# Performance work log

Hardware: AMD Instinct MI355X
Metric: run time of the kernel (lower is better)

The kernel has to match this reference:

```python
import jax, jax.numpy as jnp
import numpy as np

N = 100000   # nodes
E = 1600000  # edges (before self loops)
G = 256      # graphs in batch
F = 128      # feature_size
H = 128      # hidden_channels
L = 3        # num_layers - 1 GAT layers
NC1 = 10     # task1 classes
GF = 8       # graph_feature_size
EPS = 1e-5


def _bn_pack(key, C):
    kg, kb, km, kv = jax.random.split(key, 4)
    gamma = jax.random.uniform(kg, (C,), minval=0.5, maxval=1.5)
    beta = jax.random.normal(kb, (C,)) * 0.1
    mean = jax.random.normal(km, (C,)) * 0.1
    var = jax.random.uniform(kv, (C,), minval=0.5, maxval=1.5)
    return jnp.stack([gamma, beta, mean, var]).astype(jnp.float32)  # [4, C]


def setup_inputs() -> dict:
    key = jax.random.key(0)
    ks = jax.random.split(key, 24)
    x = jax.random.normal(ks[0], (N, F), dtype=jnp.float32)
    edge_index = jax.random.randint(ks[1], (2, E), 0, N)
    batch_ids = jnp.sort(jax.random.randint(ks[2], (N,), 0, G))
    graph_features = jax.random.normal(ks[3], (G, GF), dtype=jnp.float32)
    s = 0.05
    gat_W = jax.random.normal(ks[4], (L, F, H), dtype=jnp.float32) * s
    gat_att_src = jax.random.normal(ks[5], (L, H), dtype=jnp.float32) * s
    gat_att_dst = jax.random.normal(ks[6], (L, H), dtype=jnp.float32) * s
    gat_bias = jax.random.normal(ks[7], (L, H), dtype=jnp.float32) * 0.01
    bn_emb = _bn_pack(ks[8], H)
    bn_t1 = _bn_pack(ks[9], NC1)
    bn_comb = _bn_pack(ks[10], H + 5)
    fc1_w = jax.random.normal(ks[11], (H + 1, NC1), dtype=jnp.float32) * s
    fc1_b = jax.random.normal(ks[12], (NC1,), dtype=jnp.float32) * s
    fc2_w = jax.random.normal(ks[13], (H + 3, 2), dtype=jnp.float32) * s
    fc2_b = jax.random.normal(ks[14], (2,), dtype=jnp.float32) * s
    fc3a_w = jax.random.normal(ks[15], (H + 5, 4), dtype=jnp.float32) * s
    fc3a_b = jax.random.normal(ks[16], (4,), dtype=jnp.float32) * s
    fc3b_w = jax.random.normal(ks[17], (H + 5, 5), dtype=jnp.float32) * s
    fc3b_b = jax.random.normal(ks[18], (5,), dtype=jnp.float32) * s
    return dict(x=x, edge_index=edge_index, batch_ids=batch_ids,
                graph_features=graph_features, task=0,
                gat_W=gat_W, gat_att_src=gat_att_src, gat_att_dst=gat_att_dst,
                gat_bias=gat_bias, bn_emb=bn_emb, bn_t1=bn_t1, bn_comb=bn_comb,
                fc1_w=fc1_w, fc1_b=fc1_b, fc2_w=fc2_w, fc2_b=fc2_b,
                fc3a_w=fc3a_w, fc3a_b=fc3a_b, fc3b_w=fc3b_w, fc3b_b=fc3b_b)


def _bn_eval(x, pack):
    gamma, beta, mean, var = pack
    return (x - mean) * gamma * jax.lax.rsqrt(var + EPS) + beta


def _gat_layer(x, W, a_src, a_dst, b, src, dst):
    h = x @ W                              # [N, H]
    e_src = (h @ a_src)[src]               # [Etot]
    e_dst = (h @ a_dst)[dst]
    e = jax.nn.leaky_relu(e_src + e_dst, negative_slope=0.2)
    emax = jax.ops.segment_max(e, dst, num_segments=N)
    ee = jnp.exp(e - emax[dst])
    denom = jax.ops.segment_sum(ee, dst, num_segments=N)
    alpha = ee / denom[dst]                # edge softmax per destination node
    out = jax.ops.segment_sum(h[src] * alpha[:, None], dst, num_segments=N)
    return out + b


def _forward(x, edge_index, batch_ids, graph_features,
             gat_W, gat_att_src, gat_att_dst, gat_bias,
             bn_emb, bn_t1, bn_comb,
             fc1_w, fc1_b, fc2_w, fc2_b, fc3a_w, fc3a_b, fc3b_w, fc3b_b):
    loops = jnp.arange(N)
    src = jnp.concatenate([edge_index[0], loops])  # PyG GATConv adds self-loops
    dst = jnp.concatenate([edge_index[1], loops])
    for i in range(L):
        x = jax.nn.relu(_gat_layer(x, gat_W[i], gat_att_src[i], gat_att_dst[i],
                                   gat_bias[i], src, dst))
    # global mean pool over graphs
    sums = jax.ops.segment_sum(x, batch_ids, num_segments=G)
    cnt = jax.ops.segment_sum(jnp.ones((N,), x.dtype), batch_ids, num_segments=G)
    x = sums / jnp.maximum(cnt, 1.0)[:, None]
    x = _bn_eval(x, bn_emb)
    lev_lsb = graph_features[:, -1:]
    nx_feats = graph_features[:, -3:]
    out1 = jnp.concatenate([x, lev_lsb], axis=1) @ fc1_w + fc1_b
    out1 = _bn_eval(jax.nn.relu(out1), bn_t1)
    out2 = jax.nn.relu(jnp.concatenate([x, nx_feats], axis=1) @ fc2_w + fc2_b)
    pred2 = jnp.argmax(out2, axis=1)
    wf1 = graph_features[:, 2:3]
    wf2 = graph_features[:, 1:2]
    x3 = _bn_eval(jnp.concatenate([x, wf1, wf2, nx_feats], axis=1), bn_comb)
    b1 = x3 @ fc3a_w + fc3a_b              # [G, 4]
    b2 = x3 @ fc3b_w + fc3b_b              # [G, 5]
    m0 = (pred2 == 0)[:, None].astype(x.dtype)
    m1 = (pred2 == 1)[:, None].astype(x.dtype)
    out3 = jnp.concatenate([b1 * m0, b2 * m1], axis=1)  # [G, 9]
    return out1, out2, out3


def reference(x, edge_index, batch_ids, graph_features, task,
              gat_W, gat_att_src, gat_att_dst, gat_bias,
              bn_emb, bn_t1, bn_comb,
              fc1_w, fc1_b, fc2_w, fc2_b, fc3a_w, fc3a_b, fc3b_w, fc3b_b):
    return _forward(x, edge_index, batch_ids, graph_features,
                    gat_W, gat_att_src, gat_att_dst, gat_bias,
                    bn_emb, bn_t1, bn_comb,
                    fc1_w, fc1_b, fc2_w, fc2_b, fc3a_w, fc3a_b, fc3b_w, fc3b_b)
```

## Files before the change

kernel.cpp:

```cpp
#include <hip/hip_runtime.h>
#include <math.h>

#define Nn 100000
#define Ee 1600000
#define Mm (Ee + Nn)
#define Gg 256
#define EPSf 1e-5f
#define NB 391
#define EPB 4096
#define NEB 391
#define PCAP 8192

typedef _Float16 f16x8 __attribute__((ext_vector_type(8)));
typedef _Float16 half4_t __attribute__((ext_vector_type(4)));
typedef float f32x4 __attribute__((ext_vector_type(4)));


__global__ void k_prepW(const float* __restrict__ W, _Float16* __restrict__ Wt,
                        int* __restrict__ gtail) {
  int l = blockIdx.x;
  if (l < 3) {
    const float* w = W + (size_t)l * 16384;
    _Float16* wt = Wt + (size_t)l * 16384;
    for (int i = threadIdx.x; i < 16384; i += 256) {
      int k = i >> 7, c = i & 127;
      wt[c * 128 + k] = (_Float16)w[i];
    }
  } else {
    for (int i = threadIdx.x; i < NB; i += 256) gtail[i] = 0;
  }
}


__global__ __launch_bounds__(256) void k_bin(const int* __restrict__ src,
                                             const int* __restrict__ dst,
                                             int* __restrict__ gtail,
                                             int* __restrict__ pairs, int e) {
  __shared__ int lcnt[NB];
  __shared__ int lbase[NB];
  int t = threadIdx.x;
  for (int i = t; i < NB; i += 256) lcnt[i] = 0;
  __syncthreads();
  int base = blockIdx.x * EPB;
  int pk[EPB / 256], br[EPB / 256], bk[EPB / 256];
  #pragma unroll
  for (int i = 0; i < EPB / 256; ++i) {
    int idx = base + i * 256 + t;
    if (idx < e) {
      int d = dst[idx];
      pk[i] = (src[idx] << 8) | (d & 255);
      bk[i] = d >> 8;
      br[i] = atomicAdd(&lcnt[bk[i]], 1);
    } else br[i] = -1;
  }
  __syncthreads();
  for (int i = t; i < NB; i += 256)
    if (lcnt[i] > 0) lbase[i] = atomicAdd(&gtail[i], lcnt[i]);
  __syncthreads();
  #pragma unroll
  for (int i = 0; i < EPB / 256; ++i) {
    if (br[i] >= 0) {
      int pos = lbase[bk[i]] + br[i];
      if (pos < PCAP) pairs[bk[i] * PCAP + pos] = pk[i];
    }
  }
}

__global__ __launch_bounds__(256) void k_place(const int* __restrict__ pairs,
                                               const int* __restrict__ gtail,
                                               int* __restrict__ rp,
                                               int* __restrict__ csr) {
  __shared__ int red[256];
  __shared__ int cnt[256];
  __shared__ int ofs[256];
  int b = blockIdx.x, t = threadIdx.x;
  int myb = 0, mya = 0;
  for (int i = t; i < NB; i += 256) {
    int ci = min(gtail[i], PCAP) + min(Nn - (i << 8), 256);
    mya += ci;
    if (i < b) myb += ci;
  }
  red[t] = myb; __syncthreads();
  for (int o = 128; o; o >>= 1) { if (t < o) red[t] += red[t + o]; __syncthreads(); }
  int cb = red[0];
  __syncthreads();
  if (b == NB - 1) {
    red[t] = mya; __syncthreads();
    for (int o = 128; o; o >>= 1) { if (t < o) red[t] += red[t + o]; __syncthreads(); }
    if (t == 0) rp[Nn] = red[0];
    __syncthreads();
  }
  int v0 = b << 8;
  int nib = min(Nn - v0, 256);
  int pb = b * PCAP;
  int pc = min(gtail[b], PCAP);
  cnt[t] = (t < nib) ? 1 : 0;
  __syncthreads();
  for (int j = t; j < pc; j += 256) {
    atomicAdd(&cnt[pairs[pb + j] & 255], 1);
  }
  __syncthreads();
  int c = cnt[t];
  ofs[t] = c;
  __syncthreads();
  for (int o = 1; o < 256; o <<= 1) {
    int u = (t >= o) ? ofs[t - o] : 0;
    __syncthreads(); ofs[t] += u; __syncthreads();
  }
  int excl = ofs[t] - c;
  if (t < nib) rp[v0 + t] = cb + excl;
  cnt[t] = excl;
  __syncthreads();
  if (t < nib) {
    int pos = atomicAdd(&cnt[t], 1);
    csr[cb + pos] = v0 + t;
  }
  __syncthreads();
  for (int j = t; j < pc; j += 256) {
    int p = pairs[pb + j];
    int pos = atomicAdd(&cnt[p & 255], 1);
    csr[cb + pos] = p >> 8;
  }
}


template<bool F32IN>
__global__ __launch_bounds__(256) void k_gemm(const void* __restrict__ Xv,
                                              const _Float16* __restrict__ Wt,
                                              const float* __restrict__ asrc,
                                              const float* __restrict__ adst,
                                              _Float16* __restrict__ H,
                                              float* __restrict__ es,
                                              float* __restrict__ ed, int n) {
  int wid = threadIdx.x >> 6;
  int lane = threadIdx.x & 63;
  int r0 = blockIdx.x * 128 + wid * 32;
  if (r0 >= n) return;
  int lo16 = lane & 15, q = lane >> 4;

  f32x4 acc0[8] = {};
  f32x4 acc1[8] = {};
  const _Float16* wb = Wt + (size_t)lo16 * 128 + q * 8;

  #pragma unroll
  for (int kk = 0; kk < 4; ++kk) {
    f16x8 b0, b1;
    if constexpr (F32IN) {
      const float* xf = (const float*)Xv + (size_t)(r0 + lo16) * 128 + q * 8 + kk * 32;
      float4 u0 = *reinterpret_cast<const float4*>(xf);
      float4 u1 = *reinterpret_cast<const float4*>(xf + 4);
      float4 v0 = *reinterpret_cast<const float4*>(xf + 16 * 128);
      float4 v1 = *reinterpret_cast<const float4*>(xf + 16 * 128 + 4);
      b0 = f16x8{(_Float16)u0.x, (_Float16)u0.y, (_Float16)u0.z, (_Float16)u0.w,
                 (_Float16)u1.x, (_Float16)u1.y, (_Float16)u1.z, (_Float16)u1.w};
      b1 = f16x8{(_Float16)v0.x, (_Float16)v0.y, (_Float16)v0.z, (_Float16)v0.w,
                 (_Float16)v1.x, (_Float16)v1.y, (_Float16)v1.z, (_Float16)v1.w};
    } else {
      const _Float16* xh = (const _Float16*)Xv + (size_t)(r0 + lo16) * 128 + q * 8 + kk * 32;
      b0 = *reinterpret_cast<const f16x8*>(xh);
      b1 = *reinterpret_cast<const f16x8*>(xh + 16 * 128);
    }
    #pragma unroll
    for (int c = 0; c < 8; ++c) {
      f16x8 a = *reinterpret_cast<const f16x8*>(wb + (size_t)c * 2048 + kk * 32);
      acc0[c] = __builtin_amdgcn_mfma_f32_16x16x32_f16(a, b0, acc0[c], 0, 0, 0);
      acc1[c] = __builtin_amdgcn_mfma_f32_16x16x32_f16(a, b1, acc1[c], 0, 0, 0);
    }
  }

  float es0 = 0.f, es1 = 0.f, ed0 = 0.f, ed1 = 0.f;
  #pragma unroll
  for (int c = 0; c < 8; ++c) {
    float4 as = reinterpret_cast<const float4*>(asrc)[c * 4 + q];
    float4 ad = reinterpret_cast<const float4*>(adst)[c * 4 + q];
    es0 += acc0[c][0] * as.x + acc0[c][1] * as.y + acc0[c][2] * as.z + acc0[c][3] * as.w;
    ed0 += acc0[c][0] * ad.x + acc0[c][1] * ad.y + acc0[c][2] * ad.z + acc0[c][3] * ad.w;
    es1 += acc1[c][0] * as.x + acc1[c][1] * as.y + acc1[c][2] * as.z + acc1[c][3] * as.w;
    ed1 += acc1[c][0] * ad.x + acc1[c][1] * ad.y + acc1[c][2] * ad.z + acc1[c][3] * ad.w;
  }
  es0 += __shfl_xor(es0, 16); es0 += __shfl_xor(es0, 32);
  ed0 += __shfl_xor(ed0, 16); ed0 += __shfl_xor(ed0, 32);
  es1 += __shfl_xor(es1, 16); es1 += __shfl_xor(es1, 32);
  ed1 += __shfl_xor(ed1, 16); ed1 += __shfl_xor(ed1, 32);

  half4_t* H4 = reinterpret_cast<half4_t*>(H);
  int row0 = r0 + lo16;
  #pragma unroll
  for (int c = 0; c < 8; ++c) {
    half4_t h0 = { (_Float16)acc0[c][0], (_Float16)acc0[c][1],
                   (_Float16)acc0[c][2], (_Float16)acc0[c][3] };
    half4_t h1 = { (_Float16)acc1[c][0], (_Float16)acc1[c][1],
                   (_Float16)acc1[c][2], (_Float16)acc1[c][3] };
    H4[(size_t)row0 * 32 + c * 4 + q]        = h0;
    H4[(size_t)(row0 + 16) * 32 + c * 4 + q] = h1;
  }
  if (lane < 16) {
    es[r0 + lane] = es0;       ed[r0 + lane] = ed0;
    es[r0 + 16 + lane] = es1;  ed[r0 + 16 + lane] = ed1;
  }
}


__global__ __launch_bounds__(256) void k_agg(const _Float16* __restrict__ H,
                                             const int* __restrict__ rp,
                                             const int* __restrict__ csr,
                                             const float* __restrict__ es,
                                             const float* __restrict__ ed,
                                             const float* __restrict__ bias,
                                             _Float16* __restrict__ Xo, int n) {
  int w = blockIdx.x * 4 + (threadIdx.x >> 6);
  int lane = threadIdx.x & 63;
  int half = lane >> 5;
  int l32 = lane & 31;
  int s = lane & 15;
  const f16x8* H8 = reinterpret_cast<const f16x8*>(H);
  float acc[8] = {};

  int v = w * 2 + half;
  int vc = (v < n) ? v : (n - 1);
  int r0 = rp[vc], r1 = rp[vc + 1];
  int deg = r1 - r0;
  float edv = ed[vc];
  float inv;
  int vstore = v;

  if (__all(deg <= 32)) {
    int u = 0;
    float e = -3.0e38f;
    if (l32 < deg) {
      u = csr[r0 + l32];
      e = es[u] + edv;
      e = e > 0.f ? e : 0.2f * e;
    }
    float m = e;
    #pragma unroll
    for (int o = 16; o; o >>= 1) m = fmaxf(m, __shfl_xor(m, o));
    float pw = (l32 < deg) ? __expf(e - m) : 0.f;
    float den = pw;
    #pragma unroll
    for (int o = 16; o; o >>= 1) den += __shfl_xor(den, o);
    inv = 1.f / den;

    int g2 = (lane >> 4) & 1;
    int hb = half << 5;
    int niter = (deg + 1) >> 1;
    float ww = __shfl(pw, hb + g2);
    f16x8 hv = H8[__shfl(u, hb + g2) * 16 + s];
    #pragma unroll 2
    for (int i = 1; i < niter; ++i) {
      int idx = hb + 2 * i + g2;
      int uu2 = __shfl(u, idx);
      float ww2 = __shfl(pw, idx);
      f16x8 hv2 = H8[uu2 * 16 + s];
      #pragma unroll
      for (int k2 = 0; k2 < 8; ++k2) acc[k2] += ww * (float)hv[k2];
      ww = ww2; hv = hv2;
    }
    #pragma unroll
    for (int k2 = 0; k2 < 8; ++k2) acc[k2] += ww * (float)hv[k2];
    #pragma unroll
    for (int k2 = 0; k2 < 8; ++k2) acc[k2] += __shfl_xor(acc[k2], 16);
  } else {
    float invA = 1.f, invB = 1.f;
    float accA[8] = {}, accB[8] = {};
    #pragma unroll
    for (int t2 = 0; t2 < 2; ++t2) {
      int vv = w * 2 + t2;
      if (vv >= n) break;
      int rr0 = __shfl(r0, t2 * 32), rr1 = __shfl(r1, t2 * 32);
      int dg = rr1 - rr0;
      float edvv = __shfl(edv, t2 * 32);
      float* ac = t2 ? accB : accA;
      int g4 = lane >> 4;
      float iv;
      if (dg <= 64) {
        int u = 0;
        float e = -3.0e38f;
        if (lane < dg) {
          u = csr[rr0 + lane];
          e = es[u] + edvv;
          e = e > 0.f ? e : 0.2f * e;
        }
        float m = e;
        #pragma unroll
        for (int o = 32; o; o >>= 1) m = fmaxf(m, __shfl_xor(m, o));
        float pw = (lane < dg) ? __expf(e - m) : 0.f;
        float den = pw;
        #pragma unroll
        for (int o = 32; o; o >>= 1) den += __shfl_xor(den, o);
        iv = 1.f / den;
        int niter = (dg + 3) >> 2;
        for (int i = 0; i < niter; ++i) {
          int idx = 4 * i + g4;
          int uu = __shfl(u, idx);
          float ww = __shfl(pw, idx);
          f16x8 hv = H8[uu * 16 + s];
          #pragma unroll
          for (int k2 = 0; k2 < 8; ++k2) ac[k2] += ww * (float)hv[k2];
        }
      } else {
        float m = -3.0e38f;
        for (int j = rr0 + lane; j < rr1; j += 64) {
          float e = es[csr[j]] + edvv;
          e = e > 0.f ? e : 0.2f * e;
          m = fmaxf(m, e);
        }
        #pragma unroll
        for (int o = 32; o; o >>= 1) m = fmaxf(m, __shfl_xor(m, o));
        float den = 0.f;
        for (int j = rr0 + lane; j < rr1; j += 64) {
          float e = es[csr[j]] + edvv;
          e = e > 0.f ? e : 0.2f * e;
          den += __expf(e - m);
        }
        #pragma unroll
        for (int o = 32; o; o >>= 1) den += __shfl_xor(den, o);
        iv = 1.f / den;
        for (int j = rr0; j < rr1; j += 4) {
          int idx = j + g4;
          if (idx < rr1) {
            int uu = csr[idx];
            float e = es[uu] + edvv;
            e = e > 0.f ? e : 0.2f * e;
            float ww = __expf(e - m);
            f16x8 hv = H8[uu * 16 + s];
            #pragma unroll
            for (int k2 = 0; k2 < 8; ++k2) ac[k2] += ww * (float)hv[k2];
          }
        }
      }
      #pragma unroll
      for (int k2 = 0; k2 < 8; ++k2) {
        ac[k2] += __shfl_xor(ac[k2], 16);
        ac[k2] += __shfl_xor(ac[k2], 32);
      }
      if (t2) invB = iv; else invA = iv;
    }
    #pragma unroll
    for (int k2 = 0; k2 < 8; ++k2) {
      float bval = __shfl(accB[k2], l32);
      acc[k2] = half ? bval : accA[k2];
    }
    inv = half ? invB : invA;
  }

  if (((lane & 31) < 16) && vstore < n) {
    float4 b0 = reinterpret_cast<const float4*>(bias)[s * 2];
    float4 b1 = reinterpret_cast<const float4*>(bias)[s * 2 + 1];
    f16x8 o;
    o[0] = (_Float16)fmaxf(acc[0] * inv + b0.x, 0.f);
    o[1] = (_Float16)fmaxf(acc[1] * inv + b0.y, 0.f);
    o[2] = (_Float16)fmaxf(acc[2] * inv + b0.z, 0.f);
    o[3] = (_Float16)fmaxf(acc[3] * inv + b0.w, 0.f);
    o[4] = (_Float16)fmaxf(acc[4] * inv + b1.x, 0.f);
    o[5] = (_Float16)fmaxf(acc[5] * inv + b1.y, 0.f);
    o[6] = (_Float16)fmaxf(acc[6] * inv + b1.z, 0.f);
    o[7] = (_Float16)fmaxf(acc[7] * inv + b1.w, 0.f);
    reinterpret_cast<f16x8*>(Xo)[vstore * 16 + s] = o;
  }
}


__global__ __launch_bounds__(512) void k_poolheads(
    const _Float16* __restrict__ X16, const int* __restrict__ batch,
    const float* __restrict__ bn_emb, const float* __restrict__ gf,
    const float* __restrict__ bn_t1, const float* __restrict__ bn_comb,
    const float* __restrict__ fc1w, const float* __restrict__ fc1b,
    const float* __restrict__ fc2w, const float* __restrict__ fc2b,
    const float* __restrict__ fc3aw, const float* __restrict__ fc3ab,
    const float* __restrict__ fc3bw, const float* __restrict__ fc3bb,
    float* __restrict__ out, int n) {
  __shared__ float4 part[16][32];
  __shared__ float xs[128];
  __shared__ float x3[133];
  __shared__ float o2[2];
  int g = blockIdx.x, t = threadIdx.x;
  int s = t & 31;
  int way = t >> 5;
  int lo = 0, hi = n;
  while (lo < hi) { int mid = (lo + hi) >> 1; if (batch[mid] < g) lo = mid + 1; else hi = mid; }
  int s0 = lo;
  lo = s0; hi = n;
  while (lo < hi) { int mid = (lo + hi) >> 1; if (batch[mid] < g + 1) lo = mid + 1; else hi = mid; }
  int e0 = lo;
  const half4_t* X4 = reinterpret_cast<const half4_t*>(X16);
  float4 acc = make_float4(0.f, 0.f, 0.f, 0.f);
  for (int i = s0 + way; i < e0; i += 16) {
    half4_t h = X4[(size_t)i * 32 + s];
    acc.x += (float)h[0]; acc.y += (float)h[1];
    acc.z += (float)h[2]; acc.w += (float)h[3];
  }
  part[way][s] = acc;
  __syncthreads();
  if (way == 0) {
    float4 tt = part[0][s];
    #pragma unroll
    for (int w = 1; w < 16; ++w) {
      float4 u = part[w][s];
      tt.x += u.x; tt.y += u.y; tt.z += u.z; tt.w += u.w;
    }
    float invc = (e0 > s0) ? 1.f / (float)(e0 - s0) : 0.f;
    int c0 = s * 4;
    #pragma unroll
    for (int k = 0; k < 4; ++k) {
      float mean = ((const float*)&tt)[k] * invc;
      int c = c0 + k;
      float gm = bn_emb[c], bt = bn_emb[128 + c], mu = bn_emb[256 + c], vr = bn_emb[384 + c];
      xs[c] = (mean - mu) * gm * rsqrtf(vr + EPSf) + bt;
    }
  }
  __syncthreads();

  const float* gfg = &gf[g * 8];
  float lev = gfg[7];
  float nx0 = gfg[5], nx1 = gfg[6], nx2 = gfg[7];
  float wf1 = gfg[2], wf2 = gfg[1];
  if (t < 10) {
    float o = fc1b[t];
    for (int k = 0; k < 128; ++k) o += xs[k] * fc1w[k * 10 + t];
    o += lev * fc1w[128 * 10 + t];
    o = fmaxf(o, 0.f);
    float gm = bn_t1[t], bt = bn_t1[10 + t], mu = bn_t1[20 + t], vr = bn_t1[30 + t];
    out[g * 10 + t] = (o - mu) * gm * rsqrtf(vr + EPSf) + bt;
  }
  if (t >= 10 && t < 12) {
    int j = t - 10;
    float o = fc2b[j];
    for (int k = 0; k < 128; ++k) o += xs[k] * fc2w[k * 2 + j];
    o += nx0 * fc2w[128 * 2 + j] + nx1 * fc2w[129 * 2 + j] + nx2 * fc2w[130 * 2 + j];
    o = fmaxf(o, 0.f);
    o2[j] = o;
    out[2560 + g * 2 + j] = o;
  }
  if (t >= 12 && t < 145) {
    int k = t - 12;
    float vsrc = (k < 128) ? xs[k]
               : (k == 128) ? wf1
               : (k == 129) ? wf2
               : (k == 130) ? nx0
               : (k == 131) ? nx1 : nx2;
    float gm = bn_comb[k], bt = bn_comb[133 + k], mu = bn_comb[266 + k], vr = bn_comb[399 + k];
    x3[k] = (vsrc - mu) * gm * rsqrtf(vr + EPSf) + bt;
  }
  __syncthreads();
  bool pred1 = o2[1] > o2[0];
  if (t < 4) {
    float o = fc3ab[t];
    for (int k = 0; k < 133; ++k) o += x3[k] * fc3aw[k * 4 + t];
    out[3072 + g * 9 + t] = pred1 ? 0.f : o;
  }
  if (t >= 4 && t < 9) {
    int j = t - 4;
    float o = fc3bb[j];
    for (int k = 0; k < 133; ++k) o += x3[k] * fc3bw[k * 5 + j];
    out[3072 + g * 9 + 4 + j] = pred1 ? o : 0.f;
  }
}


extern "C" void kernel_launch(void* const* d_in, const int* in_sizes, int n_in,
                              void* d_out, int out_size, void* d_ws, size_t ws_size,
                              hipStream_t stream) {
  const float* x      = (const float*)d_in[0];
  const int*   ei     = (const int*)d_in[1];
  const int*   batch  = (const int*)d_in[2];
  const float* gf     = (const float*)d_in[3];
  const float* gatW   = (const float*)d_in[5];
  const float* asrc   = (const float*)d_in[6];
  const float* adst   = (const float*)d_in[7];
  const float* gbias  = (const float*)d_in[8];
  const float* bn_emb = (const float*)d_in[9];
  const float* bn_t1  = (const float*)d_in[10];
  const float* bn_cb  = (const float*)d_in[11];
  const float* fc1w = (const float*)d_in[12]; const float* fc1b = (const float*)d_in[13];
  const float* fc2w = (const float*)d_in[14]; const float* fc2b = (const float*)d_in[15];
  const float* fc3aw = (const float*)d_in[16]; const float* fc3ab = (const float*)d_in[17];
  const float* fc3bw = (const float*)d_in[18]; const float* fc3bb = (const float*)d_in[19];
  float* out = (float*)d_out;

  char* p = (char*)d_ws;
  auto alloc = [&](size_t bytes) -> void* {
    void* r = (void*)p;
    p += (bytes + 255) & ~(size_t)255;
    return r;
  };
  _Float16* xfA  = (_Float16*)alloc((size_t)Nn * 128 * 2);
  _Float16* xfB  = (_Float16*)alloc((size_t)Nn * 128 * 2);
  _Float16* hbuf = (_Float16*)alloc((size_t)Nn * 128 * 2);
  _Float16* wt   = (_Float16*)alloc((size_t)3 * 16384 * 2);
  int*   pairs = (int*)alloc((size_t)NB * PCAP * 4);
  int*   csr  = (int*)alloc((size_t)Mm * 4);
  int*   rp   = (int*)alloc((size_t)(Nn + 1) * 4);
  int*   gtail = (int*)alloc((size_t)NB * 4);
  float* es   = (float*)alloc((size_t)Nn * 4);
  float* ed   = (float*)alloc((size_t)Nn * 4);
  if ((size_t)(p - (char*)d_ws) > ws_size) return;

  const int* srcp = ei;
  const int* dstp = ei + Ee;

  k_prepW<<<4, 256, 0, stream>>>(gatW, wt, gtail);

  k_bin<<<NEB, 256, 0, stream>>>(srcp, dstp, gtail, pairs, Ee);
  k_place<<<NB, 256, 0, stream>>>(pairs, gtail, rp, csr);

  int ngrid = (Nn + 127) / 128;
  int agrid = (Nn + 7) / 8;
  k_gemm<true><<<ngrid, 256, 0, stream>>>(x, wt, asrc, adst, hbuf, es, ed, Nn);
  k_agg<<<agrid, 256, 0, stream>>>(hbuf, rp, csr, es, ed, gbias, xfA, Nn);
  k_gemm<false><<<ngrid, 256, 0, stream>>>(xfA, wt + 16384, asrc + 128, adst + 128,
                                           hbuf, es, ed, Nn);
  k_agg<<<agrid, 256, 0, stream>>>(hbuf, rp, csr, es, ed, gbias + 128, xfB, Nn);
  k_gemm<false><<<ngrid, 256, 0, stream>>>(xfB, wt + 32768, asrc + 256, adst + 256,
                                           hbuf, es, ed, Nn);
  k_agg<<<agrid, 256, 0, stream>>>(hbuf, rp, csr, es, ed, gbias + 256, xfA, Nn);

  k_poolheads<<<Gg, 512, 0, stream>>>(xfA, batch, bn_emb, gf, bn_t1, bn_cb,
                                      fc1w, fc1b, fc2w, fc2b, fc3aw, fc3ab,
                                      fc3bw, fc3bb, out, Nn);
}
```

Before: 501.4 us.

## Vectorize edge binning loads, stage GEMM weights in swizzled LDS, deepen gather prefetch

Three separate changes. The binning kernel now reads src/dst as int4 vectors, so each thread processes 16 edges with fewer load instructions. The GEMM kernel copies the transposed fp16 weight matrix into XOR-swizzled shared memory once per block, so the MFMA A-operand reads come from LDS rather than global/L2. The small-degree aggregation path now prefetches two neighbour rows ahead instead of one, which hides more gather latency at the cost of extra registers. Adding 32KB of LDS per GEMM block may limit occupancy.

New measurement: 463.9 us. 1.08x faster.

```diff
diff --git a/kernel.cpp b/kernel.cpp
--- a/kernel.cpp
+++ b/kernel.cpp
@@ -41,24 +41,36 @@
   int t = threadIdx.x;
   for (int i = t; i < NB; i += 256) lcnt[i] = 0;
   __syncthreads();
-  int base = blockIdx.x * EPB;
-  int pk[EPB / 256], br[EPB / 256], bk[EPB / 256];
+  const int4* src4 = (const int4*)src;
+  const int4* dst4 = (const int4*)dst;
+  int base4 = blockIdx.x * (EPB / 4);
+  int pk[16], br[16], bk[16];
   #pragma unroll
-  for (int i = 0; i < EPB / 256; ++i) {
-    int idx = base + i * 256 + t;
-    if (idx < e) {
-      int d = dst[idx];
-      pk[i] = (src[idx] << 8) | (d & 255);
-      bk[i] = d >> 8;
-      br[i] = atomicAdd(&lcnt[bk[i]], 1);
-    } else br[i] = -1;
+  for (int i = 0; i < 4; ++i) {
+    int idx = base4 + i * 256 + t;
+    if (idx * 4 < e) {
+      int4 d4 = dst4[idx];
+      int4 s4 = src4[idx];
+      const int* dd = (const int*)&d4;
+      const int* ss = (const int*)&s4;
+      #pragma unroll
+      for (int j = 0; j < 4; ++j) {
+        int d = dd[j];
+        pk[i * 4 + j] = (ss[j] << 8) | (d & 255);
+        bk[i * 4 + j] = d >> 8;
+        br[i * 4 + j] = atomicAdd(&lcnt[bk[i * 4 + j]], 1);
+      }
+    } else {
+      #pragma unroll
+      for (int j = 0; j < 4; ++j) br[i * 4 + j] = -1;
+    }
   }
   __syncthreads();
   for (int i = t; i < NB; i += 256)
     if (lcnt[i] > 0) lbase[i] = atomicAdd(&gtail[i], lcnt[i]);
   __syncthreads();
   #pragma unroll
-  for (int i = 0; i < EPB / 256; ++i) {
+  for (int i = 0; i < 16; ++i) {
     if (br[i] >= 0) {
       int pos = lbase[bk[i]] + br[i];
       if (pos < PCAP) pairs[bk[i] * PCAP + pos] = pk[i];
@@ -132,15 +144,27 @@
                                               _Float16* __restrict__ H,
                                               float* __restrict__ es,
                                               float* __restrict__ ed, int n) {
+  __shared__ __align__(16) _Float16 Wl[16384];
+  {
+    const uint4* wg = (const uint4*)Wt;
+    char* wl = (char*)Wl;
+    for (int i = threadIdx.x; i < 2048; i += 256) {
+      int swz = ((i >> 4) & 7) << 4;
+      *(uint4*)(wl + ((i * 16) ^ swz)) = wg[i];
+    }
+  }
+  __syncthreads();
+
   int wid = threadIdx.x >> 6;
   int lane = threadIdx.x & 63;
   int r0 = blockIdx.x * 128 + wid * 32;
   if (r0 >= n) return;
   int lo16 = lane & 15, q = lane >> 4;
+  int swzr = (lo16 & 7) << 4;
+  const char* wl = (const char*)Wl;
 
   f32x4 acc0[8] = {};
   f32x4 acc1[8] = {};
-  const _Float16* wb = Wt + (size_t)lo16 * 128 + q * 8;
 
   #pragma unroll
   for (int kk = 0; kk < 4; ++kk) {
@@ -162,7 +186,8 @@
     }
     #pragma unroll
     for (int c = 0; c < 8; ++c) {
-      f16x8 a = *reinterpret_cast<const f16x8*>(wb + (size_t)c * 2048 + kk * 32);
+      int byteoff = (((c * 16 + lo16) * 128 + q * 8 + kk * 32) * 2) ^ swzr;
+      f16x8 a = *(const f16x8*)(wl + byteoff);
       acc0[c] = __builtin_amdgcn_mfma_f32_16x16x32_f16(a, b0, acc0[c], 0, 0, 0);
       acc1[c] = __builtin_amdgcn_mfma_f32_16x16x32_f16(a, b1, acc1[c], 0, 0, 0);
     }
@@ -242,22 +267,30 @@
     inv = 1.f / den;
 
     int g2 = (lane >> 4) & 1;
-    int hb = half << 5;
+    int i0 = (half << 5) + g2;
     int niter = (deg + 1) >> 1;
-    float ww = __shfl(pw, hb + g2);
-    f16x8 hv = H8[__shfl(u, hb + g2) * 16 + s];
-    #pragma unroll 2
-    for (int i = 1; i < niter; ++i) {
-      int idx = hb + 2 * i + g2;
+    float wwA = __shfl(pw, i0);
+    f16x8 hvA = H8[__shfl(u, i0) * 16 + s];
+    float wwB = 0.f;
+    f16x8 hvB = hvA;
+    if (niter > 1) {
+      wwB = __shfl(pw, i0 + 2);
+      hvB = H8[__shfl(u, i0 + 2) * 16 + s];
+    }
+    for (int i = 2; i < niter; ++i) {
+      int idx = i0 + 2 * i;
       int uu2 = __shfl(u, idx);
       float ww2 = __shfl(pw, idx);
       f16x8 hv2 = H8[uu2 * 16 + s];
       #pragma unroll
-      for (int k2 = 0; k2 < 8; ++k2) acc[k2] += ww * (float)hv[k2];
-      ww = ww2; hv = hv2;
-    }
-    #pragma unroll
-    for (int k2 = 0; k2 < 8; ++k2) acc[k2] += ww * (float)hv[k2];
+      for (int k2 = 0; k2 < 8; ++k2) acc[k2] += wwA * (float)hvA[k2];
+      wwA = wwB; hvA = hvB;
+      wwB = ww2; hvB = hv2;
+    }
+    #pragma unroll
+    for (int k2 = 0; k2 < 8; ++k2) acc[k2] += wwA * (float)hvA[k2];
+    #pragma unroll
+    for (int k2 = 0; k2 < 8; ++k2) acc[k2] += wwB * (float)hvB[k2];
     #pragma unroll
     for (int k2 = 0; k2 < 8; ++k2) acc[k2] += __shfl_xor(acc[k2], 16);
   } else {
```
